# Kernel tuning notes

Hardware: AMD Instinct MI355X
Metric: run time of the kernel (lower is better)

Reference implementation:

```python
import jax, jax.numpy as jnp
import numpy as np

B, T, D, H, O = 128, 1024, 256, 512, 256

def setup_inputs() -> dict:
    key = jax.random.key(0)
    k0, k1, k2, k3 = jax.random.split(key, 4)
    s_i = 1.0 / np.sqrt(D)
    s_h = 1.0 / np.sqrt(H)
    return {
        "X": jax.random.normal(k0, (B, T, D), jnp.float32),
        "Wi": jax.random.normal(k1, (D, 4 * H), jnp.float32) * s_i,  # input kernel (no bias in flax OptimizedLSTMCell input dense)
        "Wh": jax.random.normal(k2, (H, 4 * H), jnp.float32) * s_h,  # recurrent kernel
        "b": jnp.zeros((4 * H,), jnp.float32),                        # recurrent bias
        "Wd": jax.random.normal(k3, (H, O), jnp.float32) * s_h,      # output Dense kernel
        "bd": jnp.zeros((O,), jnp.float32),                           # output Dense bias
    }

def _lstm_last_hidden(X, Wi, Wh, b):
    # Precompute input projections for all timesteps (same linear map, hoisted out of scan)
    x_proj = jnp.einsum('btd,dg->btg', X, Wi)  # [B, T, 4H]
    h_dim = Wh.shape[0]
    c0 = jnp.zeros((X.shape[0], h_dim), X.dtype)
    h0 = c0

    def step(carry, xt):
        c, h = carry
        y = xt + h @ Wh + b  # [B, 4H]
        i, f, g, o = jnp.split(y, 4, axis=-1)  # flax OptimizedLSTMCell gate order: i, f, g, o
        i = jax.nn.sigmoid(i)
        f = jax.nn.sigmoid(f)
        g = jnp.tanh(g)
        o = jax.nn.sigmoid(o)
        c_new = f * c + i * g
        h_new = o * jnp.tanh(c_new)
        return (c_new, h_new), None

    (c_T, h_T), _ = jax.lax.scan(step, (c0, h0), jnp.swapaxes(x_proj, 0, 1))
    return h_T  # [B, H] = last hidden state

def reference(X, Wi, Wh, b, Wd, bd):
    # Original applies Dense to all timesteps then slices [:, -1, :];
    # Dense is pointwise over time, so applying it to the last hidden is identical math.
    h_last = _lstm_last_hidden(X, Wi, Wh, b)
    return h_last @ Wd + bd  # [B, O]
```

## Files before the change

kernel.cpp:

```cpp
#include <hip/hip_runtime.h>
#include <hip/hip_bf16.h>

#define Bb 128
#define Tt 1024
#define Dd 256
#define Hh 512
#define G4 2048
#define Oo 256

#define NBG 8
#define WPB 16
#define NWG_LAUNCH 256
#define BLOCK 512

#define SPIN_CAP (1u << 16)

typedef __attribute__((ext_vector_type(8))) short short8;
typedef __attribute__((ext_vector_type(4))) float f32x4;
typedef unsigned long long u64;

#define TICK_OFF 0
#define CNT_OFF  2048
#define HBUF_OFF 4096
#define WS_ZERO_BYTES (4096 + Bb*Hh*2)

__device__ __forceinline__ short f2bf(float f) {
  __hip_bfloat16 h = __float2bfloat16(f);
  return *reinterpret_cast<short*>(&h);
}
__device__ __forceinline__ float sigm(float x) {
  return __builtin_amdgcn_rcpf(1.f + __expf(-x));
}
__device__ __forceinline__ float tanh_(float x) {
  return fmaf(2.f, __builtin_amdgcn_rcpf(1.f + __expf(-2.f * x)), -1.f);
}

#define MFMA16(A, B, C) __builtin_amdgcn_mfma_f32_16x16x32_bf16((A), (B), (C), 0, 0, 0)

__global__ __launch_bounds__(BLOCK, 2) void lstm_seq(
    const float* __restrict__ X, const float* __restrict__ Wi,
    const float* __restrict__ Wh, const float* __restrict__ bias,
    char* hbuf, int* cnts, int* tickets)
{
  __shared__ char sH[16 * 1024];
  __shared__ char sX[16 * 512];
  __shared__ unsigned short hstage[16][40];
  __shared__ int sSlot;

  const int tid  = threadIdx.x;
  const int w    = tid >> 6;
  const int lane = tid & 63;

  int myxcc;
  asm volatile("s_getreg_b32 %0, hwreg(HW_REG_XCC_ID)" : "=s"(myxcc));
  myxcc &= 7;
  if (tid == 0) {
    sSlot = __hip_atomic_fetch_add(&tickets[myxcc * 16], 1,
                                   __ATOMIC_RELAXED, __HIP_MEMORY_SCOPE_AGENT);
  }
  __syncthreads();
  const int gjw = sSlot;
  if (gjw >= WPB) return;
  const int bg = myxcc;
  int* cnt = cnts + bg * 32;

  const int cjj  = lane & 15;
  const int kgrp = lane >> 4;
  const int gate = cjj >> 2;
  const int c4   = cjj & 3;
  const int colg = gate * Hh + gjw * 32 + w * 4 + c4;

  short8 wf[24];
#pragma unroll
  for (int kk = 0; kk < 24; ++kk) {
    short8 f;
#pragma unroll
    for (int i = 0; i < 8; ++i) {
      int k = kk * 32 + kgrp * 8 + i;
      float v = (k < Hh) ? Wh[(size_t)k * G4 + colg]
                         : Wi[(size_t)(k - Hh) * G4 + colg];
      f[i] = f2bf(v);
    }
    wf[kk] = f;
  }
  const float bvv = bias[colg];

  const int arow = cjj;
  const int aswz = (arow & 7) << 4;
  float cpr[4] = {0.f, 0.f, 0.f, 0.f};

  const int hc0 = (tid + gjw * 64) & 1023;
  const int hc1 = (tid + 512 + gjw * 64) & 1023;
  const int hrow0 = hc0 >> 6, hoff0 = hc0 & 63;
  const int hrow1 = hc1 >> 6, hoff1 = hc1 & 63;

  const int xrow = tid >> 5, xseg = tid & 31;
  const float* xbase = X + (size_t)(bg * 16 + xrow) * Tt * Dd + xseg * 8;
  f32x4 xA0 = *reinterpret_cast<const f32x4*>(xbase);
  f32x4 xA1 = *reinterpret_cast<const f32x4*>(xbase + 4);
  f32x4 xB0 = *reinterpret_cast<const f32x4*>(xbase + Dd);
  f32x4 xB1 = *reinterpret_cast<const f32x4*>(xbase + Dd + 4);

  auto STEP = [&](int s, f32x4& xv0, f32x4& xv1) {
    const char* hread  = hbuf + (size_t)((s - 1) & 1) * (Bb * Hh * 2);
    char*       hwrite = hbuf + (size_t)(s & 1) * (Bb * Hh * 2);

    {
      short8 xb;
      xb[0] = f2bf(xv0[0]); xb[1] = f2bf(xv0[1]); xb[2] = f2bf(xv0[2]); xb[3] = f2bf(xv0[3]);
      xb[4] = f2bf(xv1[0]); xb[5] = f2bf(xv1[1]); xb[6] = f2bf(xv1[2]); xb[7] = f2bf(xv1[3]);
      *reinterpret_cast<short8*>(sX + xrow * 512 + ((xseg * 16) ^ ((xrow & 7) << 4))) = xb;
    }
    __syncthreads();

    f32x4 acc_a, acc_b;
#pragma unroll
    for (int m = 0; m < 4; ++m) { acc_a[m] = bvv; acc_b[m] = 0.f; }
#pragma unroll
    for (int kk = 0; kk < 4; ++kk) {
      short8 a = *reinterpret_cast<const short8*>(
          sX + arow * 512 + ((kk * 64 + kgrp * 16) ^ aswz));
      acc_a = MFMA16(a, wf[16 + kk], acc_a);
    }
#pragma unroll
    for (int kk = 4; kk < 8; ++kk) {
      short8 a = *reinterpret_cast<const short8*>(
          sX + arow * 512 + ((kk * 64 + kgrp * 16) ^ aswz));
      acc_b = MFMA16(a, wf[16 + kk], acc_b);
    }

    if (s > 1 && tid == 0) {
      const int tgt = WPB * (s - 1);
      unsigned spin = 0;
      while ((int)(__hip_atomic_fetch_add((unsigned*)cnt, 0x10000u,
                                          __ATOMIC_RELAXED,
                                          __HIP_MEMORY_SCOPE_WORKGROUP) & 0xFFFFu) < tgt
             && ++spin < SPIN_CAP) {
        __builtin_amdgcn_s_sleep(1);
      }
    }
    __syncthreads();

    asm volatile("buffer_inv sc0" ::: "memory");
    {
      f32x4 v0 = *reinterpret_cast<const f32x4*>(
          hread + (size_t)(bg * 16 + hrow0) * 1024 + hoff0 * 16);
      f32x4 v1 = *reinterpret_cast<const f32x4*>(
          hread + (size_t)(bg * 16 + hrow1) * 1024 + hoff1 * 16);
      *reinterpret_cast<f32x4*>(
          sH + hrow0 * 1024 + ((hoff0 * 16) ^ ((hrow0 & 7) << 4))) = v0;
      *reinterpret_cast<f32x4*>(
          sH + hrow1 * 1024 + ((hoff1 * 16) ^ ((hrow1 & 7) << 4))) = v1;
    }
    __syncthreads();

#pragma unroll
    for (int kk = 0; kk < 8; ++kk) {
      short8 a = *reinterpret_cast<const short8*>(
          sH + arow * 1024 + ((kk * 64 + kgrp * 16) ^ aswz));
      acc_a = MFMA16(a, wf[kk], acc_a);
    }
#pragma unroll
    for (int kk = 8; kk < 16; ++kk) {
      short8 a = *reinterpret_cast<const short8*>(
          sH + arow * 1024 + ((kk * 64 + kgrp * 16) ^ aswz));
      acc_b = MFMA16(a, wf[kk], acc_b);
    }
    f32x4 acc;
#pragma unroll
    for (int m = 0; m < 4; ++m) acc[m] = acc_a[m] + acc_b[m];

    float r1[4], r2[4], r3[4];
#pragma unroll
    for (int m = 0; m < 4; ++m) {
      r1[m] = __shfl_xor(acc[m], 4);
      r2[m] = __shfl_xor(acc[m], 8);
      r3[m] = __shfl_xor(r1[m], 8);
    }
    if (cjj < 4) {
#pragma unroll
      for (int m = 0; m < 4; ++m) {
        float ig = sigm(acc[m]), fg = sigm(r1[m]);
        float gg = tanh_(r2[m]), og = sigm(r3[m]);
        float c = fg * cpr[m] + ig * gg;
        cpr[m] = c;
        float hh = og * tanh_(c);
        __hip_bfloat16 hb = __float2bfloat16(hh);
        hstage[kgrp * 4 + m][w * 4 + c4] = *reinterpret_cast<unsigned short*>(&hb);
      }
    }
    __syncthreads();

    if (tid < 64) {
      int row = tid >> 2, chunk = tid & 3;
      f32x4 v = *reinterpret_cast<const f32x4*>(&hstage[row][chunk * 8]);
      *reinterpret_cast<f32x4*>(
          hwrite + ((size_t)(bg * 16 + row) * Hh + gjw * 32 + chunk * 8) * 2) = v;
      asm volatile("s_waitcnt vmcnt(0)" ::: "memory");
      if (tid == 0) {
        (void)__hip_atomic_fetch_add(cnt, 1, __ATOMIC_RELAXED,
                                     __HIP_MEMORY_SCOPE_WORKGROUP);
      }
    }

    if (s + 2 <= Tt) {
      xv0 = *reinterpret_cast<const f32x4*>(xbase + (size_t)(s + 1) * Dd);
      xv1 = *reinterpret_cast<const f32x4*>(xbase + (size_t)(s + 1) * Dd + 4);
    }
  };

  for (int s = 1; s <= Tt; s += 2) {
    STEP(s,     xA0, xA1);
    STEP(s + 1, xB0, xB1);
  }
}

__global__ void out_dense(const __hip_bfloat16* __restrict__ hT,
                          const float* __restrict__ Wd,
                          const float* __restrict__ bd,
                          float* __restrict__ out)
{
  __shared__ float hrow[Hh];
  int b = blockIdx.x;
  int o = threadIdx.x;
  for (int k = o; k < Hh; k += Oo)
    hrow[k] = __bfloat162float(hT[(size_t)b * Hh + k]);
  __syncthreads();
  float acc = bd[o];
  for (int k = 0; k < Hh; ++k)
    acc = fmaf(hrow[k], Wd[(size_t)k * Oo + o], acc);
  out[(size_t)b * Oo + o] = acc;
}

extern "C" void kernel_launch(void* const* d_in, const int* in_sizes, int n_in,
                              void* d_out, int out_size, void* d_ws, size_t ws_size,
                              hipStream_t stream) {
  (void)in_sizes; (void)n_in; (void)out_size; (void)ws_size;
  const float* X  = (const float*)d_in[0];
  const float* Wi = (const float*)d_in[1];
  const float* Wh = (const float*)d_in[2];
  const float* b  = (const float*)d_in[3];
  const float* Wd = (const float*)d_in[4];
  const float* bd = (const float*)d_in[5];
  float* out = (float*)d_out;

  char* ws = (char*)d_ws;
  int* tickets = (int*)(ws + TICK_OFF);
  int* cnts    = (int*)(ws + CNT_OFF);
  char* hbuf   = ws + HBUF_OFF;

  hipMemsetAsync(d_ws, 0, WS_ZERO_BYTES, stream);
  lstm_seq<<<NWG_LAUNCH, BLOCK, 0, stream>>>(X, Wi, Wh, b, hbuf, cnts, tickets);
  out_dense<<<Bb, Oo, 0, stream>>>((const __hip_bfloat16*)hbuf, Wd, bd, out);
}
```

Measured before the change: 2.524 ms.

## Halve workgroups per batch group, each computing two column tiles per wave

Each batch group now uses 8 workgroups instead of 16. Every wave handles 8 hidden units, which means two 16-column MFMA tiles and twice the register-resident weight fragments. Gate extraction changes to one shuffle per tile, with the i/g and f/o pairs split across the two tiles. The aim is to shrink the set of workgroups taking part in the per-step cross-workgroup barrier, so synchronisation latency drops. In exchange each workgroup does twice the MFMA work per step and needs twice the weight registers, which may spill or cut occupancy.

```diff
diff --git a/kernel.cpp b/kernel.cpp
--- a/kernel.cpp
+++ b/kernel.cpp
@@ -9,8 +9,8 @@
 #define Oo 256
 
 #define NBG 8
-#define WPB 16
-#define NWG_LAUNCH 256
+#define WPB 8
+#define NWG_LAUNCH 128
 #define BLOCK 512
 
 #define SPIN_CAP (1u << 16)
@@ -44,7 +44,7 @@
 {
   __shared__ char sH[16 * 1024];
   __shared__ char sX[16 * 512];
-  __shared__ unsigned short hstage[16][40];
+  __shared__ unsigned short hstage[16][72];
   __shared__ int sSlot;
 
   const int tid  = threadIdx.x;
@@ -66,31 +66,35 @@
 
   const int cjj  = lane & 15;
   const int kgrp = lane >> 4;
-  const int gate = cjj >> 2;
-  const int c4   = cjj & 3;
-  const int colg = gate * Hh + gjw * 32 + w * 4 + c4;
-
-  short8 wf[24];
-#pragma unroll
-  for (int kk = 0; kk < 24; ++kk) {
-    short8 f;
-#pragma unroll
-    for (int i = 0; i < 8; ++i) {
-      int k = kk * 32 + kgrp * 8 + i;
-      float v = (k < Hh) ? Wh[(size_t)k * G4 + colg]
-                         : Wi[(size_t)(k - Hh) * G4 + colg];
-      f[i] = f2bf(v);
-    }
-    wf[kk] = f;
+  short8 wf[2][24];
+  float bv[2];
+#pragma unroll
+  for (int nt = 0; nt < 2; ++nt) {
+    int c = nt * 16 + cjj;
+    int gate = c >> 3, jj0 = c & 7;
+    int colg = gate * Hh + gjw * 64 + w * 8 + jj0;
+    bv[nt] = bias[colg];
+#pragma unroll
+    for (int kk = 0; kk < 24; ++kk) {
+      short8 f;
+#pragma unroll
+      for (int i = 0; i < 8; ++i) {
+        int k = kk * 32 + kgrp * 8 + i;
+        float v = (k < Hh) ? Wh[(size_t)k * G4 + colg]
+                           : Wi[(size_t)(k - Hh) * G4 + colg];
+        f[i] = f2bf(v);
+      }
+      wf[nt][kk] = f;
+    }
   }
-  const float bvv = bias[colg];
 
   const int arow = cjj;
   const int aswz = (arow & 7) << 4;
+  const int ejj  = cjj & 7;
   float cpr[4] = {0.f, 0.f, 0.f, 0.f};
 
-  const int hc0 = (tid + gjw * 64) & 1023;
-  const int hc1 = (tid + 512 + gjw * 64) & 1023;
+  const int hc0 = (tid + gjw * 128) & 1023;
+  const int hc1 = (tid + 512 + gjw * 128) & 1023;
   const int hrow0 = hc0 >> 6, hoff0 = hc0 & 63;
   const int hrow1 = hc1 >> 6, hoff1 = hc1 & 63;
 
@@ -113,20 +117,24 @@
     }
     __syncthreads();
 
-    f32x4 acc_a, acc_b;
-#pragma unroll
-    for (int m = 0; m < 4; ++m) { acc_a[m] = bvv; acc_b[m] = 0.f; }
+    f32x4 a0a, a0b, a1a, a1b;
+#pragma unroll
+    for (int m = 0; m < 4; ++m) {
+      a0a[m] = bv[0]; a0b[m] = 0.f; a1a[m] = bv[1]; a1b[m] = 0.f;
+    }
 #pragma unroll
     for (int kk = 0; kk < 4; ++kk) {
       short8 a = *reinterpret_cast<const short8*>(
           sX + arow * 512 + ((kk * 64 + kgrp * 16) ^ aswz));
-      acc_a = MFMA16(a, wf[16 + kk], acc_a);
+      a0a = MFMA16(a, wf[0][16 + kk], a0a);
+      a1a = MFMA16(a, wf[1][16 + kk], a1a);
     }
 #pragma unroll
     for (int kk = 4; kk < 8; ++kk) {
       short8 a = *reinterpret_cast<const short8*>(
           sX + arow * 512 + ((kk * 64 + kgrp * 16) ^ aswz));
-      acc_b = MFMA16(a, wf[16 + kk], acc_b);
+      a0b = MFMA16(a, wf[0][16 + kk], a0b);
+      a1b = MFMA16(a, wf[1][16 + kk], a1b);
     }
 
     if (s > 1 && tid == 0) {
@@ -158,44 +166,51 @@
     for (int kk = 0; kk < 8; ++kk) {
       short8 a = *reinterpret_cast<const short8*>(
           sH + arow * 1024 + ((kk * 64 + kgrp * 16) ^ aswz));
-      acc_a = MFMA16(a, wf[kk], acc_a);
+      a0a = MFMA16(a, wf[0][kk], a0a);
+      a1a = MFMA16(a, wf[1][kk], a1a);
     }
 #pragma unroll
     for (int kk = 8; kk < 16; ++kk) {
       short8 a = *reinterpret_cast<const short8*>(
           sH + arow * 1024 + ((kk * 64 + kgrp * 16) ^ aswz));
-      acc_b = MFMA16(a, wf[kk], acc_b);
-    }
-    f32x4 acc;
-#pragma unroll
-    for (int m = 0; m < 4; ++m) acc[m] = acc_a[m] + acc_b[m];
-
-    float r1[4], r2[4], r3[4];
+      a0b = MFMA16(a, wf[0][kk], a0b);
+      a1b = MFMA16(a, wf[1][kk], a1b);
+    }
+    f32x4 acc0, acc1;
 #pragma unroll
     for (int m = 0; m < 4; ++m) {
-      r1[m] = __shfl_xor(acc[m], 4);
-      r2[m] = __shfl_xor(acc[m], 8);
-      r3[m] = __shfl_xor(r1[m], 8);
-    }
-    if (cjj < 4) {
+      acc0[m] = a0a[m] + a0b[m];
+      acc1[m] = a1a[m] + a1b[m];
+    }
+
+    float o0[4], o1[4];
+#pragma unroll
+    for (int m = 0; m < 4; ++m) {
+      o0[m] = __shfl_xor(acc0[m], 8);
+      o1[m] = __shfl_xor(acc1[m], 8);
+    }
+    if (cjj < 8) {
 #pragma unroll
       for (int m = 0; m < 4; ++m) {
-        float ig = sigm(acc[m]), fg = sigm(r1[m]);
-        float gg = tanh_(r2[m]), og = sigm(r3[m]);
+        float ig = sigm(acc0[m]), fg = sigm(o0[m]);
+        float gg = tanh_(acc1[m]), og = sigm(o1[m]);
         float c = fg * cpr[m] + ig * gg;
         cpr[m] = c;
         float hh = og * tanh_(c);
         __hip_bfloat16 hb = __float2bfloat16(hh);
-        hstage[kgrp * 4 + m][w * 4 + c4] = *reinterpret_cast<unsigned short*>(&hb);
+        hstage[kgrp * 4 + m][w * 8 + ejj] = *reinterpret_cast<unsigned short*>(&hb);
       }
     }
     __syncthreads();
 
     if (tid < 64) {
-      int row = tid >> 2, chunk = tid & 3;
-      f32x4 v = *reinterpret_cast<const f32x4*>(&hstage[row][chunk * 8]);
-      *reinterpret_cast<f32x4*>(
-          hwrite + ((size_t)(bg * 16 + row) * Hh + gjw * 32 + chunk * 8) * 2) = v;
+      int row = tid >> 2, cp = tid & 3;
+      const char* src = reinterpret_cast<const char*>(&hstage[row][0]) + cp * 32;
+      f32x4 v0 = *reinterpret_cast<const f32x4*>(src);
+      f32x4 v1 = *reinterpret_cast<const f32x4*>(src + 16);
+      char* dst = hwrite + ((size_t)(bg * 16 + row) * Hh + gjw * 64 + cp * 16) * 2;
+      *reinterpret_cast<f32x4*>(dst) = v0;
+      *reinterpret_cast<f32x4*>(dst + 16) = v1;
       asm volatile("s_waitcnt vmcnt(0)" ::: "memory");
       if (tid == 0) {
         (void)__hip_atomic_fetch_add(cnt, 1, __ATOMIC_RELAXED,
```

After: 5.075 ms. 2.01x slower.
